# Kernel optimization log

Hardware: AMD Instinct MI355X
Metric: run time of the kernel (lower is better)

## Reference

```python
import jax, jax.numpy as jnp
import numpy as np

B, N, D = 16, 2048, 512   # batch, tokens, latent dim
K = 8192                  # codebook size


def setup_inputs() -> dict:
    key = jax.random.key(0)
    k1, k2 = jax.random.split(key)
    ze = jax.random.normal(k1, (B, N, D), dtype=jnp.float32)
    codebook = jax.random.normal(k2, (K, D), dtype=jnp.float32)
    return {"ze": ze, "codebook": codebook}


def reference(ze, codebook):
    # Pairwise squared distances: ||ze||^2 + ||c||^2 - 2 ze.c  -> [B, N, K]
    sq_norm = (
        jnp.sum(ze ** 2, axis=-1, keepdims=True)
        + jnp.sum(codebook ** 2, axis=1)
        - 2.0 * jnp.einsum("bnd,kd->bnk", ze, codebook)
    )
    argmin = jnp.argmin(sq_norm, axis=-1)  # [B, N]
    zq = codebook[argmin]                  # gather -> [B, N, D]
    return zq
```

## Files before the change

### kernel.cpp

```cpp
#include <hip/hip_runtime.h>
#include <cfloat>

#define TOKENS 32768
#define DDIM   512
#define KCODES 8192

#define CAP    160
#define MARGIN 2.0f

#define ZEBF_OFF   0
#define CBBF_OFF   (TOKENS * DDIM * 2)
#define CNORM_OFF  (CBBF_OFF + KCODES * DDIM * 2)
#define CNT_OFF    (CNORM_OFF + KCODES * 4)
#define CANDI_OFF  (CNT_OFF + TOKENS * 4)
#define CANDS_OFF  (CANDI_OFF + TOKENS * CAP * 4)
#define WS_REQ     ((size_t)(CANDS_OFF + TOKENS * CAP * 4))

typedef short bf16x8 __attribute__((ext_vector_type(8)));
typedef float f32x4  __attribute__((ext_vector_type(4)));

__device__ __forceinline__ void gld16(const void* g, void* l) {
    __builtin_amdgcn_global_load_lds(
        (const __attribute__((address_space(1))) void*)g,
        (__attribute__((address_space(3))) void*)l,
        16, 0, 0);
}

__device__ __forceinline__ unsigned short f2bf(float f) {
    union { float f; unsigned int u; } v; v.f = f;
    unsigned int u = v.u;
    return (unsigned short)((u + 0x7fffu + ((u >> 16) & 1u)) >> 16);
}

__global__ __launch_bounds__(256) void convert_kernel(const float* __restrict__ src,
                                                      unsigned short* __restrict__ dst,
                                                      int n8) {
    int i = blockIdx.x * 256 + threadIdx.x;
    if (i >= n8) return;
    float4 a = ((const float4*)src)[i * 2];
    float4 b = ((const float4*)src)[i * 2 + 1];
    bf16x8 o;
    o[0] = (short)f2bf(a.x); o[1] = (short)f2bf(a.y);
    o[2] = (short)f2bf(a.z); o[3] = (short)f2bf(a.w);
    o[4] = (short)f2bf(b.x); o[5] = (short)f2bf(b.y);
    o[6] = (short)f2bf(b.z); o[7] = (short)f2bf(b.w);
    *(bf16x8*)&dst[(size_t)i * 8] = o;
}

__global__ __launch_bounds__(256) void cnorm_kernel(const float* __restrict__ cb,
                                                    float* __restrict__ cnorm) {
    int row  = blockIdx.x * 4 + (threadIdx.x >> 6);
    int lane = threadIdx.x & 63;
    const float* r = cb + (size_t)row * DDIM;
    float s = 0.f;
    #pragma unroll
    for (int d = lane; d < DDIM; d += 64) { float v = r[d]; s += v * v; }
    #pragma unroll
    for (int off = 32; off > 0; off >>= 1) s += __shfl_down(s, off, 64);
    if (lane == 0) cnorm[row] = s;
}

__global__ __launch_bounds__(256, 2) void vq_mfma_kernel(
        const unsigned short* __restrict__ zebf,
        const unsigned short* __restrict__ cbbf,
        const float* __restrict__ cnorm,
        int* __restrict__ cnt,
        int* __restrict__ candI,
        float* __restrict__ candS) {
    __shared__ unsigned short Ab[256 * 64];
    __shared__ unsigned short Bb[128 * 64];

    const int tid  = threadIdx.x;
    const int w    = tid >> 6;
    const int lane = tid & 63;
    const int tok0  = blockIdx.y * 256;
    const int code0 = blockIdx.x * 128;

    f32x4 acc[4][8];
    const f32x4 zero = {0.f, 0.f, 0.f, 0.f};
    #pragma unroll
    for (int i = 0; i < 4; ++i)
        #pragma unroll
        for (int j = 0; j < 8; ++j) acc[i][j] = zero;

    for (int dk = 0; dk < DDIM; dk += 64) {
        __syncthreads();
        #pragma unroll
        for (int i = 0; i < 8; ++i) {
            int L    = ((i * 4 + w) * 1024) + lane * 16;
            int row  = L >> 7;
            int phys = (L >> 4) & 7;
            int slog = phys ^ (row & 7);
            gld16(zebf + (size_t)(tok0 + row) * DDIM + dk + slog * 8, (char*)Ab + L);
            if (i < 4)
                gld16(cbbf + (size_t)(code0 + row) * DDIM + dk + slog * 8, (char*)Bb + L);
        }
        __syncthreads();

        #pragma unroll
        for (int kk = 0; kk < 2; ++kk) {
            bf16x8 af[4], bfr[8];
            int slog = kk * 4 + (lane >> 4);
            #pragma unroll
            for (int rt = 0; rt < 4; ++rt) {
                int row  = w * 64 + rt * 16 + (lane & 15);
                int phys = slog ^ (row & 7);
                af[rt] = *(const bf16x8*)(Ab + row * 64 + phys * 8);
            }
            #pragma unroll
            for (int ct = 0; ct < 8; ++ct) {
                int row  = ct * 16 + (lane & 15);
                int phys = slog ^ (row & 7);
                bfr[ct] = *(const bf16x8*)(Bb + row * 64 + phys * 8);
            }
            #pragma unroll
            for (int rt = 0; rt < 4; ++rt)
                #pragma unroll
                for (int ct = 0; ct < 8; ++ct)
                    acc[rt][ct] = __builtin_amdgcn_mfma_f32_16x16x32_bf16(
                        af[rt], bfr[ct], acc[rt][ct], 0, 0, 0);
        }
    }

    float cn[8];
    #pragma unroll
    for (int ct = 0; ct < 8; ++ct)
        cn[ct] = cnorm[code0 + ct * 16 + (lane & 15)];

    #pragma unroll
    for (int rt = 0; rt < 4; ++rt)
        #pragma unroll
        for (int r = 0; r < 4; ++r) {
            float m = cn[0] - 2.f * acc[rt][0][r];
            #pragma unroll
            for (int ct = 1; ct < 8; ++ct)
                m = fminf(m, cn[ct] - 2.f * acc[rt][ct][r]);
            #pragma unroll
            for (int off = 1; off < 16; off <<= 1)
                m = fminf(m, __shfl_xor(m, off, 64));
            float thr = m + MARGIN;

            int token = tok0 + w * 64 + rt * 16 + (lane >> 4) * 4 + r;
            #pragma unroll
            for (int ct = 0; ct < 8; ++ct) {
                float s = cn[ct] - 2.f * acc[rt][ct][r];
                if (s <= thr) {
                    int pos = atomicAdd(&cnt[token], 1);
                    if (pos < CAP) {
                        candI[(size_t)token * CAP + pos] = code0 + ct * 16 + (lane & 15);
                        candS[(size_t)token * CAP + pos] = s;
                    }
                }
            }
        }
}

__global__ __launch_bounds__(64) void rescore_kernel(
        const float* __restrict__ ze, const float* __restrict__ cb,
        const float* __restrict__ cnorm, const int* __restrict__ cnt,
        const int* __restrict__ candI, const float* __restrict__ candS,
        float* __restrict__ out) {
    const int t    = blockIdx.x;
    const int lane = threadIdx.x;

    float4 za = *(const float4*)&ze[(size_t)t * DDIM + lane * 8];
    float4 zb = *(const float4*)&ze[(size_t)t * DDIM + lane * 8 + 4];

    int n = cnt[t];
    bool ovf = (n > CAP) || (n <= 0);

    float best = FLT_MAX;
    int   bidx = 0x7fffffff;

    if (!ovf) {
        float m = FLT_MAX;
        for (int e = lane; e < n; e += 64)
            m = fminf(m, candS[(size_t)t * CAP + e]);
        #pragma unroll
        for (int off = 32; off > 0; off >>= 1)
            m = fminf(m, __shfl_xor(m, off, 64));
        float thr = m + MARGIN;

        for (int base = 0; base < n; base += 64) {
            int e = base + lane;
            int myI = 0; float sv = FLT_MAX;
            if (e < n) { myI = candI[(size_t)t * CAP + e]; sv = candS[(size_t)t * CAP + e]; }
            unsigned long long mask = __ballot(e < n && sv <= thr);
            while (mask) {
                int b = __ffsll((long long)mask) - 1;
                mask &= mask - 1;
                int code = __shfl(myI, b, 64);
                const float* row = cb + (size_t)code * DDIM + lane * 8;
                float4 ca = *(const float4*)row;
                float4 cc = *(const float4*)(row + 4);
                float d = za.x*ca.x + za.y*ca.y + za.z*ca.z + za.w*ca.w
                        + zb.x*cc.x + zb.y*cc.y + zb.z*cc.z + zb.w*cc.w;
                #pragma unroll
                for (int off = 32; off > 0; off >>= 1) d += __shfl_xor(d, off, 64);
                float s = cnorm[code] - 2.f * d;
                if (s < best || (s == best && code < bidx)) { best = s; bidx = code; }
            }
        }
    } else {
        for (int code = 0; code < KCODES; ++code) {
            const float* row = cb + (size_t)code * DDIM + lane * 8;
            float4 ca = *(const float4*)row;
            float4 cc = *(const float4*)(row + 4);
            float d = za.x*ca.x + za.y*ca.y + za.z*ca.z + za.w*ca.w
                    + zb.x*cc.x + zb.y*cc.y + zb.z*cc.z + zb.w*cc.w;
            #pragma unroll
            for (int off = 32; off > 0; off >>= 1) d += __shfl_xor(d, off, 64);
            float s = cnorm[code] - 2.f * d;
            if (s < best || (s == best && code < bidx)) { best = s; bidx = code; }
        }
    }

    const float* src = cb + (size_t)bidx * DDIM + lane * 8;
    float4 o0 = *(const float4*)src;
    float4 o1 = *(const float4*)(src + 4);
    *(float4*)&out[(size_t)t * DDIM + lane * 8]     = o0;
    *(float4*)&out[(size_t)t * DDIM + lane * 8 + 4] = o1;
}

#define TM 64
#define TN 64
#define BK 32
#define LDS_STRIDE (TM + 4)

__global__ __launch_bounds__(256) void vq_fallback_kernel(const float* __restrict__ ze,
                                                          const float* __restrict__ cb,
                                                          const float* __restrict__ cnorm,
                                                          float* __restrict__ out) {
    __shared__ float At[BK][LDS_STRIDE];
    __shared__ float Bt[BK][LDS_STRIDE];
    __shared__ float rv[TM][16];
    __shared__ int   ri[TM][16];
    __shared__ int   best_s[TM];

    const int tid = threadIdx.x;
    const int tx  = tid & 15;
    const int ty  = tid >> 4;
    const int token_base = blockIdx.x * TM;
    const int sc = tid & 31;
    const int sr = tid >> 5;

    float bestv[4] = {FLT_MAX, FLT_MAX, FLT_MAX, FLT_MAX};
    int   besti[4] = {0, 0, 0, 0};

    for (int ctile = 0; ctile < KCODES; ctile += TN) {
        float acc[4][4] = {{0.f}};
        for (int dk = 0; dk < DDIM; dk += BK) {
            __syncthreads();
            #pragma unroll
            for (int p = 0; p < 8; ++p) {
                int r = p * 8 + sr;
                At[sc][r] = ze[(size_t)(token_base + r) * DDIM + dk + sc];
                Bt[sc][r] = cb[(size_t)(ctile + r) * DDIM + dk + sc];
            }
            __syncthreads();
            #pragma unroll
            for (int d = 0; d < BK; ++d) {
                float a[4], b[4];
                *(float4*)a = *(const float4*)&At[d][ty * 4];
                *(float4*)b = *(const float4*)&Bt[d][tx * 4];
                #pragma unroll
                for (int i = 0; i < 4; ++i)
                    #pragma unroll
                    for (int j = 0; j < 4; ++j)
                        acc[i][j] += a[i] * b[j];
            }
        }
        #pragma unroll
        for (int j = 0; j < 4; ++j) {
            int code = ctile + tx * 4 + j;
            float cnv = cnorm[code];
            #pragma unroll
            for (int i = 0; i < 4; ++i) {
                float s = cnv - 2.f * acc[i][j];
                if (s < bestv[i]) { bestv[i] = s; besti[i] = code; }
            }
        }
    }
    #pragma unroll
    for (int i = 0; i < 4; ++i) {
        rv[ty * 4 + i][tx] = bestv[i];
        ri[ty * 4 + i][tx] = besti[i];
    }
    __syncthreads();
    if (tid < TM) {
        float bv = rv[tid][0]; int bi = ri[tid][0];
        #pragma unroll
        for (int x = 1; x < 16; ++x) {
            float v = rv[tid][x]; int ix = ri[tid][x];
            if (v < bv || (v == bv && ix < bi)) { bv = v; bi = ix; }
        }
        best_s[tid] = bi;
    }
    __syncthreads();
    const int gr   = tid >> 7;
    const int gcol = (tid & 127) * 4;
    for (int rr = 0; rr < TM; rr += 2) {
        int tk  = rr + gr;
        int src = best_s[tk];
        float4 v = *(const float4*)&cb[(size_t)src * DDIM + gcol];
        *(float4*)&out[(size_t)(token_base + tk) * DDIM + gcol] = v;
    }
}

extern "C" void kernel_launch(void* const* d_in, const int* in_sizes, int n_in,
                              void* d_out, int out_size, void* d_ws, size_t ws_size,
                              hipStream_t stream) {
    const float* ze = (const float*)d_in[0];
    const float* cb = (const float*)d_in[1];
    float* out      = (float*)d_out;

    if (ws_size < WS_REQ) {
        float* cnorm = (float*)d_ws;
        cnorm_kernel<<<KCODES / 4, 256, 0, stream>>>(cb, cnorm);
        vq_fallback_kernel<<<TOKENS / TM, 256, 0, stream>>>(ze, cb, cnorm, out);
        return;
    }

    char* ws = (char*)d_ws;
    unsigned short* zebf = (unsigned short*)(ws + ZEBF_OFF);
    unsigned short* cbbf = (unsigned short*)(ws + CBBF_OFF);
    float* cnorm = (float*)(ws + CNORM_OFF);
    int*   cnt   = (int*)(ws + CNT_OFF);
    int*   candI = (int*)(ws + CANDI_OFF);
    float* candS = (float*)(ws + CANDS_OFF);

    convert_kernel<<<(TOKENS * DDIM / 8) / 256, 256, 0, stream>>>(ze, zebf, TOKENS * DDIM / 8);
    convert_kernel<<<(KCODES * DDIM / 8) / 256, 256, 0, stream>>>(cb, cbbf, KCODES * DDIM / 8);
    cnorm_kernel<<<KCODES / 4, 256, 0, stream>>>(cb, cnorm);
    hipMemsetAsync(cnt, 0, TOKENS * sizeof(int), stream);

    dim3 grid(KCODES / 128, TOKENS / 256);
    vq_mfma_kernel<<<grid, 256, 0, stream>>>(zebf, cbbf, cnorm, cnt, candI, candS);

    rescore_kernel<<<TOKENS, 64, 0, stream>>>(ze, cb, cnorm, cnt, candI, candS, out);
}
```

Baseline: 832.3 us.

## Load MFMA fragments directly from global memory with register double-buffering

Removes the LDS staging and the two block barriers per k-step in the main MFMA GEMM. Each wave now loads its bf16 A and B fragments straight from global memory into registers, double-buffered so the next k-slice loads while the current MFMA batch runs. This drops LDS traffic and synchronisation, but each of the 4 waves now fetches the same B tile separately, relying on the cache. It also adds register pressure and gives up coalesced row loads under the 256,2 launch bound.

```diff
diff --git a/kernel.cpp b/kernel.cpp
--- a/kernel.cpp
+++ b/kernel.cpp
@@ -18,13 +18,6 @@
 
 typedef short bf16x8 __attribute__((ext_vector_type(8)));
 typedef float f32x4  __attribute__((ext_vector_type(4)));
-
-__device__ __forceinline__ void gld16(const void* g, void* l) {
-    __builtin_amdgcn_global_load_lds(
-        (const __attribute__((address_space(1))) void*)g,
-        (__attribute__((address_space(3))) void*)l,
-        16, 0, 0);
-}
 
 __device__ __forceinline__ unsigned short f2bf(float f) {
     union { float f; unsigned int u; } v; v.f = f;
@@ -60,6 +53,27 @@
     if (lane == 0) cnorm[row] = s;
 }
 
+__device__ __forceinline__ void load_frags(const unsigned short* __restrict__ aB,
+                                           const unsigned short* __restrict__ bB,
+                                           int ko, bf16x8* af, bf16x8* bfr) {
+    #pragma unroll
+    for (int rt = 0; rt < 4; ++rt)
+        af[rt] = *(const bf16x8*)(aB + (size_t)rt * 16 * DDIM + ko);
+    #pragma unroll
+    for (int ct = 0; ct < 8; ++ct)
+        bfr[ct] = *(const bf16x8*)(bB + (size_t)ct * 16 * DDIM + ko);
+}
+
+__device__ __forceinline__ void mfma_step(const bf16x8* af, const bf16x8* bfr,
+                                          f32x4 acc[4][8]) {
+    #pragma unroll
+    for (int rt = 0; rt < 4; ++rt)
+        #pragma unroll
+        for (int ct = 0; ct < 8; ++ct)
+            acc[rt][ct] = __builtin_amdgcn_mfma_f32_16x16x32_bf16(
+                af[rt], bfr[ct], acc[rt][ct], 0, 0, 0);
+}
+
 __global__ __launch_bounds__(256, 2) void vq_mfma_kernel(
         const unsigned short* __restrict__ zebf,
         const unsigned short* __restrict__ cbbf,
@@ -67,14 +81,14 @@
         int* __restrict__ cnt,
         int* __restrict__ candI,
         float* __restrict__ candS) {
-    __shared__ unsigned short Ab[256 * 64];
-    __shared__ unsigned short Bb[128 * 64];
-
     const int tid  = threadIdx.x;
     const int w    = tid >> 6;
     const int lane = tid & 63;
-    const int tok0  = blockIdx.y * 256;
+    const int tok0  = blockIdx.y * 256 + w * 64;
     const int code0 = blockIdx.x * 128;
+
+    const unsigned short* aB = zebf + (size_t)(tok0  + (lane & 15)) * DDIM + (lane >> 4) * 8;
+    const unsigned short* bB = cbbf + (size_t)(code0 + (lane & 15)) * DDIM + (lane >> 4) * 8;
 
     f32x4 acc[4][8];
     const f32x4 zero = {0.f, 0.f, 0.f, 0.f};
@@ -83,43 +97,16 @@
         #pragma unroll
         for (int j = 0; j < 8; ++j) acc[i][j] = zero;
 
+    bf16x8 afA[4], bfA[8], afB[4], bfB[8];
+    load_frags(aB, bB, 0, afA, bfA);
+
+    #pragma unroll
     for (int dk = 0; dk < DDIM; dk += 64) {
-        __syncthreads();
-        #pragma unroll
-        for (int i = 0; i < 8; ++i) {
-            int L    = ((i * 4 + w) * 1024) + lane * 16;
-            int row  = L >> 7;
-            int phys = (L >> 4) & 7;
-            int slog = phys ^ (row & 7);
-            gld16(zebf + (size_t)(tok0 + row) * DDIM + dk + slog * 8, (char*)Ab + L);
-            if (i < 4)
-                gld16(cbbf + (size_t)(code0 + row) * DDIM + dk + slog * 8, (char*)Bb + L);
-        }
-        __syncthreads();
-
-        #pragma unroll
-        for (int kk = 0; kk < 2; ++kk) {
-            bf16x8 af[4], bfr[8];
-            int slog = kk * 4 + (lane >> 4);
-            #pragma unroll
-            for (int rt = 0; rt < 4; ++rt) {
-                int row  = w * 64 + rt * 16 + (lane & 15);
-                int phys = slog ^ (row & 7);
-                af[rt] = *(const bf16x8*)(Ab + row * 64 + phys * 8);
-            }
-            #pragma unroll
-            for (int ct = 0; ct < 8; ++ct) {
-                int row  = ct * 16 + (lane & 15);
-                int phys = slog ^ (row & 7);
-                bfr[ct] = *(const bf16x8*)(Bb + row * 64 + phys * 8);
-            }
-            #pragma unroll
-            for (int rt = 0; rt < 4; ++rt)
-                #pragma unroll
-                for (int ct = 0; ct < 8; ++ct)
-                    acc[rt][ct] = __builtin_amdgcn_mfma_f32_16x16x32_bf16(
-                        af[rt], bfr[ct], acc[rt][ct], 0, 0, 0);
-        }
+        load_frags(aB, bB, dk + 32, afB, bfB);
+        mfma_step(afA, bfA, acc);
+        if (dk + 64 < DDIM)
+            load_frags(aB, bB, dk + 64, afA, bfA);
+        mfma_step(afB, bfB, acc);
     }
 
     float cn[8];
@@ -140,7 +127,7 @@
                 m = fminf(m, __shfl_xor(m, off, 64));
             float thr = m + MARGIN;
 
-            int token = tok0 + w * 64 + rt * 16 + (lane >> 4) * 4 + r;
+            int token = tok0 + rt * 16 + (lane >> 4) * 4 + r;
             #pragma unroll
             for (int ct = 0; ct < 8; ++ct) {
                 float s = cn[ct] - 2.f * acc[rt][ct][r];
```

New measurement: 1.246 ms. +49.7%, slower.
